# Kernel optimization log

Hardware: AMD Instinct MI355X
Metric: run time of the kernel (lower is better)

The kernel has to match this reference:

```python
import jax, jax.numpy as jnp
import numpy as np


def _gru_cell(x, h, wih, whh, bih, bhh):
    """PyTorch GRUCell semantics. x:[B,2] h:[B,2] wih/whh:[6,2] bih/bhh:[6]."""
    gi = x @ wih.T + bih  # [B,6]
    gh = h @ whh.T + bhh  # [B,6]
    i_r, i_z, i_n = jnp.split(gi, 3, axis=1)
    h_r, h_z, h_n = jnp.split(gh, 3, axis=1)
    r = jax.nn.sigmoid(i_r + h_r)
    z = jax.nn.sigmoid(i_z + h_z)
    n = jnp.tanh(i_n + r * h_n)
    return (1.0 - z) * n + z * h


def setup_inputs() -> dict:
    key = jax.random.key(0)
    ks = jax.random.split(key, 13)
    B = 1048576
    s = 0.5  # small init scale for stable gates
    return {
        "x": jax.random.normal(ks[0], (B, 19), dtype=jnp.float32),
        "up_wih": jax.random.normal(ks[1], (6, 2), dtype=jnp.float32) * s,
        "up_whh": jax.random.normal(ks[2], (6, 2), dtype=jnp.float32) * s,
        "up_bih": jax.random.normal(ks[3], (6,), dtype=jnp.float32) * s,
        "up_bhh": jax.random.normal(ks[4], (6,), dtype=jnp.float32) * s,
        "down_wih": jax.random.normal(ks[5], (6, 2), dtype=jnp.float32) * s,
        "down_whh": jax.random.normal(ks[6], (6, 2), dtype=jnp.float32) * s,
        "down_bih": jax.random.normal(ks[7], (6,), dtype=jnp.float32) * s,
        "down_bhh": jax.random.normal(ks[8], (6,), dtype=jnp.float32) * s,
        "obs_w": jax.random.normal(ks[9], (2, 7), dtype=jnp.float32) * s,
        "obs_b": jax.random.normal(ks[10], (2,), dtype=jnp.float32) * s,
        "out_w": jax.random.normal(ks[11], (1, 2), dtype=jnp.float32) * s,
        "out_b": jax.random.normal(ks[12], (1,), dtype=jnp.float32) * s,
    }


def reference(x, up_wih, up_whh, up_bih, up_bhh,
              down_wih, down_whh, down_bih, down_bhh,
              obs_w, obs_b, out_w, out_b):
    B = x.shape[0]
    obs = x[:, :5]                       # [B,5]
    j = x[:, 5:12]                       # [B,7]
    jd = x[:, 12:19]                     # [B,7]
    jcat = jnp.stack([j, jd], axis=-1)   # [B,7,2] per-joint (pos, vel)
    steps = jnp.swapaxes(jcat, 0, 1)     # [7,B,2]

    # up pass: scan r_up over the 7 joints, collecting hidden states
    h0 = jnp.zeros((B, 2), dtype=x.dtype)

    def up_step(h, inp):
        h_new = _gru_cell(inp, h, up_wih, up_whh, up_bih, up_bhh)
        return h_new, h_new

    h_last, h_up = jax.lax.scan(up_step, h0, steps)  # h_up: [7,B,2]

    # mix observation with final up hidden state
    h = jnp.concatenate([obs, h_last], axis=1) @ obs_w.T + obs_b  # [B,2]

    # down pass: scan r_down over stored up states, emitting actions
    def down_step(h, hu):
        h_new = _gru_cell(hu, h, down_wih, down_whh, down_bih, down_bhh)
        act = h_new @ out_w.T + out_b  # [B,1]
        return h_new, act

    _, acts = jax.lax.scan(down_step, h, h_up)  # [7,B,1]
    return jnp.swapaxes(acts, 0, 1)  # [B,7,1]
```

## Files before the change

kernel.cpp:

```cpp
#include <hip/hip_runtime.h>

#define TPB 256
#define RPB 512

__device__ __forceinline__ float ex2(float x) { return __builtin_amdgcn_exp2f(x); }
__device__ __forceinline__ float frcp(float x) { return __builtin_amdgcn_rcpf(x); }

__device__ __forceinline__ float sigm(float x) {
  return frcp(1.0f + ex2(-1.4426950408889634f * x));
}
__device__ __forceinline__ float ftanh(float x) {
  return fmaf(-2.0f, frcp(ex2(2.8853900817779268f * x) + 1.0f), 1.0f);
}

struct GruW {
  float w0, w1, w2, w3, w4, w5, w6, w7, w8, w9, w10, w11;
  float u0, u1, u2, u3, u4, u5, u6, u7, u8, u9, u10, u11;
  float br0, br1, bz0, bz1;
  float bin0, bin1, bhn0, bhn1;
};

__device__ __forceinline__ GruW load_gru(const float* __restrict__ wih,
                                         const float* __restrict__ whh,
                                         const float* __restrict__ bih,
                                         const float* __restrict__ bhh) {
  GruW g;
  g.w0 = wih[0];  g.w1 = wih[1];  g.w2 = wih[2];  g.w3 = wih[3];
  g.w4 = wih[4];  g.w5 = wih[5];  g.w6 = wih[6];  g.w7 = wih[7];
  g.w8 = wih[8];  g.w9 = wih[9];  g.w10 = wih[10]; g.w11 = wih[11];
  g.u0 = whh[0];  g.u1 = whh[1];  g.u2 = whh[2];  g.u3 = whh[3];
  g.u4 = whh[4];  g.u5 = whh[5];  g.u6 = whh[6];  g.u7 = whh[7];
  g.u8 = whh[8];  g.u9 = whh[9];  g.u10 = whh[10]; g.u11 = whh[11];
  g.br0 = bih[0] + bhh[0]; g.br1 = bih[1] + bhh[1];
  g.bz0 = bih[2] + bhh[2]; g.bz1 = bih[3] + bhh[3];
  g.bin0 = bih[4]; g.bin1 = bih[5];
  g.bhn0 = bhh[4]; g.bhn1 = bhh[5];
  return g;
}

__device__ __forceinline__ void cell(const GruW& g, float x0, float x1,
                                     float& h0, float& h1) {
  float r0 = sigm(fmaf(g.w0, x0, fmaf(g.w1, x1, fmaf(g.u0, h0, fmaf(g.u1, h1, g.br0)))));
  float r1 = sigm(fmaf(g.w2, x0, fmaf(g.w3, x1, fmaf(g.u2, h0, fmaf(g.u3, h1, g.br1)))));
  float z0 = sigm(fmaf(g.w4, x0, fmaf(g.w5, x1, fmaf(g.u4, h0, fmaf(g.u5, h1, g.bz0)))));
  float z1 = sigm(fmaf(g.w6, x0, fmaf(g.w7, x1, fmaf(g.u6, h0, fmaf(g.u7, h1, g.bz1)))));
  float gin0 = fmaf(g.w8, x0, fmaf(g.w9, x1, g.bin0));
  float gin1 = fmaf(g.w10, x0, fmaf(g.w11, x1, g.bin1));
  float ghn0 = fmaf(g.u8, h0, fmaf(g.u9, h1, g.bhn0));
  float ghn1 = fmaf(g.u10, h0, fmaf(g.u11, h1, g.bhn1));
  float n0 = ftanh(fmaf(r0, ghn0, gin0));
  float n1 = ftanh(fmaf(r1, ghn1, gin1));
  h0 = fmaf(z0, h0 - n0, n0);
  h1 = fmaf(z1, h1 - n1, n1);
}

__device__ __forceinline__ void row_compute(
    const float* __restrict__ xr, const GruW& up, const GruW& dn,
    float ow0, float ow1, float ow2, float ow3, float ow4, float ow5, float ow6,
    float ow7, float ow8, float ow9, float ow10, float ow11, float ow12, float ow13,
    float ob0, float ob1, float vw0, float vw1, float vb,
    float& o0, float& o1, float& o2, float& o3, float& o4, float& o5, float& o6) {
  float h0 = 0.f, h1 = 0.f;
  float hu0, hu1, hu2, hu3, hu4, hu5, hu6, hu7, hu8, hu9, hu10, hu11, hu12, hu13;
  cell(up, xr[5],  xr[12], h0, h1); hu0 = h0;  hu1 = h1;
  cell(up, xr[6],  xr[13], h0, h1); hu2 = h0;  hu3 = h1;
  cell(up, xr[7],  xr[14], h0, h1); hu4 = h0;  hu5 = h1;
  cell(up, xr[8],  xr[15], h0, h1); hu6 = h0;  hu7 = h1;
  cell(up, xr[9],  xr[16], h0, h1); hu8 = h0;  hu9 = h1;
  cell(up, xr[10], xr[17], h0, h1); hu10 = h0; hu11 = h1;
  cell(up, xr[11], xr[18], h0, h1); hu12 = h0; hu13 = h1;

  float a0 = fmaf(xr[0], ow0, fmaf(xr[1], ow1, fmaf(xr[2], ow2, fmaf(xr[3], ow3,
             fmaf(xr[4], ow4, fmaf(hu12, ow5, fmaf(hu13, ow6, ob0)))))));
  float a1 = fmaf(xr[0], ow7, fmaf(xr[1], ow8, fmaf(xr[2], ow9, fmaf(xr[3], ow10,
             fmaf(xr[4], ow11, fmaf(hu12, ow12, fmaf(hu13, ow13, ob1)))))));
  h0 = a0; h1 = a1;

  cell(dn, hu0,  hu1,  h0, h1); o0 = fmaf(vw0, h0, fmaf(vw1, h1, vb));
  cell(dn, hu2,  hu3,  h0, h1); o1 = fmaf(vw0, h0, fmaf(vw1, h1, vb));
  cell(dn, hu4,  hu5,  h0, h1); o2 = fmaf(vw0, h0, fmaf(vw1, h1, vb));
  cell(dn, hu6,  hu7,  h0, h1); o3 = fmaf(vw0, h0, fmaf(vw1, h1, vb));
  cell(dn, hu8,  hu9,  h0, h1); o4 = fmaf(vw0, h0, fmaf(vw1, h1, vb));
  cell(dn, hu10, hu11, h0, h1); o5 = fmaf(vw0, h0, fmaf(vw1, h1, vb));
  cell(dn, hu12, hu13, h0, h1); o6 = fmaf(vw0, h0, fmaf(vw1, h1, vb));
}

__global__ __launch_bounds__(TPB, 4) void rec_policy_kernel(
    const float* __restrict__ x,
    const float* __restrict__ up_wih, const float* __restrict__ up_whh,
    const float* __restrict__ up_bih, const float* __restrict__ up_bhh,
    const float* __restrict__ down_wih, const float* __restrict__ down_whh,
    const float* __restrict__ down_bih, const float* __restrict__ down_bhh,
    const float* __restrict__ obs_w, const float* __restrict__ obs_b,
    const float* __restrict__ out_w, const float* __restrict__ out_b,
    float* __restrict__ out, int B) {
  __shared__ __align__(16) float sx[RPB * 19];

  const int tid = threadIdx.x;
  const long base = (long)blockIdx.x * RPB;
  const int rows = min((long)RPB, (long)B - base);

  const GruW up = load_gru(up_wih, up_whh, up_bih, up_bhh);
  const GruW dn = load_gru(down_wih, down_whh, down_bih, down_bhh);
  const float ow0 = obs_w[0], ow1 = obs_w[1], ow2 = obs_w[2], ow3 = obs_w[3],
              ow4 = obs_w[4], ow5 = obs_w[5], ow6 = obs_w[6], ow7 = obs_w[7],
              ow8 = obs_w[8], ow9 = obs_w[9], ow10 = obs_w[10], ow11 = obs_w[11],
              ow12 = obs_w[12], ow13 = obs_w[13];
  const float ob0 = obs_b[0], ob1 = obs_b[1];
  const float vw0 = out_w[0], vw1 = out_w[1], vb = out_b[0];

  if (rows == RPB) {
    {
      const float4* src = (const float4*)(x + base * 19);
      float4* dst = (float4*)sx;
      for (int i = tid; i < RPB * 19 / 4; i += TPB) dst[i] = src[i];
    }
    __syncthreads();

    const float* xa = sx + tid * 19;
    const float* xb = sx + (tid + TPB) * 19;
    float ao0, ao1, ao2, ao3, ao4, ao5, ao6;
    float bo0, bo1, bo2, bo3, bo4, bo5, bo6;
    row_compute(xa, up, dn, ow0, ow1, ow2, ow3, ow4, ow5, ow6, ow7, ow8, ow9,
                ow10, ow11, ow12, ow13, ob0, ob1, vw0, vw1, vb,
                ao0, ao1, ao2, ao3, ao4, ao5, ao6);
    row_compute(xb, up, dn, ow0, ow1, ow2, ow3, ow4, ow5, ow6, ow7, ow8, ow9,
                ow10, ow11, ow12, ow13, ob0, ob1, vw0, vw1, vb,
                bo0, bo1, bo2, bo3, bo4, bo5, bo6);

    __syncthreads();
    float* soa = sx + tid * 7;
    soa[0] = ao0; soa[1] = ao1; soa[2] = ao2; soa[3] = ao3;
    soa[4] = ao4; soa[5] = ao5; soa[6] = ao6;
    float* sob = sx + (tid + TPB) * 7;
    sob[0] = bo0; sob[1] = bo1; sob[2] = bo2; sob[3] = bo3;
    sob[4] = bo4; sob[5] = bo5; sob[6] = bo6;
    __syncthreads();

    float4* dst = (float4*)(out + base * 7);
    const float4* s4 = (const float4*)sx;
    for (int i = tid; i < RPB * 7 / 4; i += TPB) dst[i] = s4[i];
  } else {
    for (int i = tid; i < rows * 19; i += TPB) sx[i] = x[base * 19 + i];
    __syncthreads();
    for (int r = tid; r < rows; r += TPB) {
      const float* xr = sx + r * 19;
      float o0, o1, o2, o3, o4, o5, o6;
      row_compute(xr, up, dn, ow0, ow1, ow2, ow3, ow4, ow5, ow6, ow7, ow8, ow9,
                  ow10, ow11, ow12, ow13, ob0, ob1, vw0, vw1, vb,
                  o0, o1, o2, o3, o4, o5, o6);
      float* po = out + (base + r) * 7;
      po[0] = o0; po[1] = o1; po[2] = o2; po[3] = o3;
      po[4] = o4; po[5] = o5; po[6] = o6;
    }
  }
}

extern "C" void kernel_launch(void* const* d_in, const int* in_sizes, int n_in,
                              void* d_out, int out_size, void* d_ws, size_t ws_size,
                              hipStream_t stream) {
  const float* x        = (const float*)d_in[0];
  const float* up_wih   = (const float*)d_in[1];
  const float* up_whh   = (const float*)d_in[2];
  const float* up_bih   = (const float*)d_in[3];
  const float* up_bhh   = (const float*)d_in[4];
  const float* down_wih = (const float*)d_in[5];
  const float* down_whh = (const float*)d_in[6];
  const float* down_bih = (const float*)d_in[7];
  const float* down_bhh = (const float*)d_in[8];
  const float* obs_w    = (const float*)d_in[9];
  const float* obs_b    = (const float*)d_in[10];
  const float* out_w    = (const float*)d_in[11];
  const float* out_b    = (const float*)d_in[12];
  float* out = (float*)d_out;

  const int B = in_sizes[0] / 19;
  const int blocks = (B + RPB - 1) / RPB;
  rec_policy_kernel<<<blocks, TPB, 0, stream>>>(
      x, up_wih, up_whh, up_bih, up_bhh, down_wih, down_whh, down_bih, down_bhh,
      obs_w, obs_b, out_w, out_b, out, B);
}
```

Measured before the change: 156.1 us.

## Drop shared-memory staging; one row per thread with direct global loads

Removes the LDS staging of input rows and outputs, along with the block barriers. Each thread now handles a single row and reads its 19 floats straight from global memory with strided scalar loads, then writes its 7 outputs directly. The launch bound is raised to 8 blocks per CU and the grid doubles. This trades coalesced float4 transfers for uncoalesced strided accesses that depend on the caches, in exchange for fewer barriers and higher occupancy.

Result: no change. 156.3 us (+0.1%).

```diff
diff --git a/kernel.cpp b/kernel.cpp
--- a/kernel.cpp
+++ b/kernel.cpp
@@ -1,7 +1,6 @@
 #include <hip/hip_runtime.h>
 
 #define TPB 256
-#define RPB 512
 
 __device__ __forceinline__ float ex2(float x) { return __builtin_amdgcn_exp2f(x); }
 __device__ __forceinline__ float frcp(float x) { return __builtin_amdgcn_rcpf(x); }
@@ -54,38 +53,7 @@
   h1 = fmaf(z1, h1 - n1, n1);
 }
 
-__device__ __forceinline__ void row_compute(
-    const float* __restrict__ xr, const GruW& up, const GruW& dn,
-    float ow0, float ow1, float ow2, float ow3, float ow4, float ow5, float ow6,
-    float ow7, float ow8, float ow9, float ow10, float ow11, float ow12, float ow13,
-    float ob0, float ob1, float vw0, float vw1, float vb,
-    float& o0, float& o1, float& o2, float& o3, float& o4, float& o5, float& o6) {
-  float h0 = 0.f, h1 = 0.f;
-  float hu0, hu1, hu2, hu3, hu4, hu5, hu6, hu7, hu8, hu9, hu10, hu11, hu12, hu13;
-  cell(up, xr[5],  xr[12], h0, h1); hu0 = h0;  hu1 = h1;
-  cell(up, xr[6],  xr[13], h0, h1); hu2 = h0;  hu3 = h1;
-  cell(up, xr[7],  xr[14], h0, h1); hu4 = h0;  hu5 = h1;
-  cell(up, xr[8],  xr[15], h0, h1); hu6 = h0;  hu7 = h1;
-  cell(up, xr[9],  xr[16], h0, h1); hu8 = h0;  hu9 = h1;
-  cell(up, xr[10], xr[17], h0, h1); hu10 = h0; hu11 = h1;
-  cell(up, xr[11], xr[18], h0, h1); hu12 = h0; hu13 = h1;
-
-  float a0 = fmaf(xr[0], ow0, fmaf(xr[1], ow1, fmaf(xr[2], ow2, fmaf(xr[3], ow3,
-             fmaf(xr[4], ow4, fmaf(hu12, ow5, fmaf(hu13, ow6, ob0)))))));
-  float a1 = fmaf(xr[0], ow7, fmaf(xr[1], ow8, fmaf(xr[2], ow9, fmaf(xr[3], ow10,
-             fmaf(xr[4], ow11, fmaf(hu12, ow12, fmaf(hu13, ow13, ob1)))))));
-  h0 = a0; h1 = a1;
-
-  cell(dn, hu0,  hu1,  h0, h1); o0 = fmaf(vw0, h0, fmaf(vw1, h1, vb));
-  cell(dn, hu2,  hu3,  h0, h1); o1 = fmaf(vw0, h0, fmaf(vw1, h1, vb));
-  cell(dn, hu4,  hu5,  h0, h1); o2 = fmaf(vw0, h0, fmaf(vw1, h1, vb));
-  cell(dn, hu6,  hu7,  h0, h1); o3 = fmaf(vw0, h0, fmaf(vw1, h1, vb));
-  cell(dn, hu8,  hu9,  h0, h1); o4 = fmaf(vw0, h0, fmaf(vw1, h1, vb));
-  cell(dn, hu10, hu11, h0, h1); o5 = fmaf(vw0, h0, fmaf(vw1, h1, vb));
-  cell(dn, hu12, hu13, h0, h1); o6 = fmaf(vw0, h0, fmaf(vw1, h1, vb));
-}
-
-__global__ __launch_bounds__(TPB, 4) void rec_policy_kernel(
+__global__ __launch_bounds__(TPB, 8) void rec_policy_kernel(
     const float* __restrict__ x,
     const float* __restrict__ up_wih, const float* __restrict__ up_whh,
     const float* __restrict__ up_bih, const float* __restrict__ up_bhh,
@@ -94,11 +62,8 @@
     const float* __restrict__ obs_w, const float* __restrict__ obs_b,
     const float* __restrict__ out_w, const float* __restrict__ out_b,
     float* __restrict__ out, int B) {
-  __shared__ __align__(16) float sx[RPB * 19];
-
-  const int tid = threadIdx.x;
-  const long base = (long)blockIdx.x * RPB;
-  const int rows = min((long)RPB, (long)B - base);
+  const long row = (long)blockIdx.x * TPB + threadIdx.x;
+  if (row >= B) return;
 
   const GruW up = load_gru(up_wih, up_whh, up_bih, up_bhh);
   const GruW dn = load_gru(down_wih, down_whh, down_bih, down_bhh);
@@ -109,51 +74,39 @@
   const float ob0 = obs_b[0], ob1 = obs_b[1];
   const float vw0 = out_w[0], vw1 = out_w[1], vb = out_b[0];
 
-  if (rows == RPB) {
-    {
-      const float4* src = (const float4*)(x + base * 19);
-      float4* dst = (float4*)sx;
-      for (int i = tid; i < RPB * 19 / 4; i += TPB) dst[i] = src[i];
-    }
-    __syncthreads();
+  const float* __restrict__ xp = x + row * 19;
+  float xr0 = xp[0],  xr1 = xp[1],  xr2 = xp[2],  xr3 = xp[3],  xr4 = xp[4];
+  float xr5 = xp[5],  xr6 = xp[6],  xr7 = xp[7],  xr8 = xp[8],  xr9 = xp[9];
+  float xr10 = xp[10], xr11 = xp[11], xr12 = xp[12], xr13 = xp[13];
+  float xr14 = xp[14], xr15 = xp[15], xr16 = xp[16], xr17 = xp[17], xr18 = xp[18];
 
-    const float* xa = sx + tid * 19;
-    const float* xb = sx + (tid + TPB) * 19;
-    float ao0, ao1, ao2, ao3, ao4, ao5, ao6;
-    float bo0, bo1, bo2, bo3, bo4, bo5, bo6;
-    row_compute(xa, up, dn, ow0, ow1, ow2, ow3, ow4, ow5, ow6, ow7, ow8, ow9,
-                ow10, ow11, ow12, ow13, ob0, ob1, vw0, vw1, vb,
-                ao0, ao1, ao2, ao3, ao4, ao5, ao6);
-    row_compute(xb, up, dn, ow0, ow1, ow2, ow3, ow4, ow5, ow6, ow7, ow8, ow9,
-                ow10, ow11, ow12, ow13, ob0, ob1, vw0, vw1, vb,
-                bo0, bo1, bo2, bo3, bo4, bo5, bo6);
+  float h0 = 0.f, h1 = 0.f;
+  float hu0, hu1, hu2, hu3, hu4, hu5, hu6, hu7, hu8, hu9, hu10, hu11, hu12, hu13;
+  cell(up, xr5,  xr12, h0, h1); hu0 = h0;  hu1 = h1;
+  cell(up, xr6,  xr13, h0, h1); hu2 = h0;  hu3 = h1;
+  cell(up, xr7,  xr14, h0, h1); hu4 = h0;  hu5 = h1;
+  cell(up, xr8,  xr15, h0, h1); hu6 = h0;  hu7 = h1;
+  cell(up, xr9,  xr16, h0, h1); hu8 = h0;  hu9 = h1;
+  cell(up, xr10, xr17, h0, h1); hu10 = h0; hu11 = h1;
+  cell(up, xr11, xr18, h0, h1); hu12 = h0; hu13 = h1;
 
-    __syncthreads();
-    float* soa = sx + tid * 7;
-    soa[0] = ao0; soa[1] = ao1; soa[2] = ao2; soa[3] = ao3;
-    soa[4] = ao4; soa[5] = ao5; soa[6] = ao6;
-    float* sob = sx + (tid + TPB) * 7;
-    sob[0] = bo0; sob[1] = bo1; sob[2] = bo2; sob[3] = bo3;
-    sob[4] = bo4; sob[5] = bo5; sob[6] = bo6;
-    __syncthreads();
+  float a0 = fmaf(xr0, ow0, fmaf(xr1, ow1, fmaf(xr2, ow2, fmaf(xr3, ow3,
+             fmaf(xr4, ow4, fmaf(hu12, ow5, fmaf(hu13, ow6, ob0)))))));
+  float a1 = fmaf(xr0, ow7, fmaf(xr1, ow8, fmaf(xr2, ow9, fmaf(xr3, ow10,
+             fmaf(xr4, ow11, fmaf(hu12, ow12, fmaf(hu13, ow13, ob1)))))));
+  h0 = a0; h1 = a1;
 
-    float4* dst = (float4*)(out + base * 7);
-    const float4* s4 = (const float4*)sx;
-    for (int i = tid; i < RPB * 7 / 4; i += TPB) dst[i] = s4[i];
-  } else {
-    for (int i = tid; i < rows * 19; i += TPB) sx[i] = x[base * 19 + i];
-    __syncthreads();
-    for (int r = tid; r < rows; r += TPB) {
-      const float* xr = sx + r * 19;
-      float o0, o1, o2, o3, o4, o5, o6;
-      row_compute(xr, up, dn, ow0, ow1, ow2, ow3, ow4, ow5, ow6, ow7, ow8, ow9,
-                  ow10, ow11, ow12, ow13, ob0, ob1, vw0, vw1, vb,
-                  o0, o1, o2, o3, o4, o5, o6);
-      float* po = out + (base + r) * 7;
-      po[0] = o0; po[1] = o1; po[2] = o2; po[3] = o3;
-      po[4] = o4; po[5] = o5; po[6] = o6;
-    }
-  }
+  float* __restrict__ po = out + row * 7;
+  float o0, o1, o2, o3, o4, o5, o6;
+  cell(dn, hu0,  hu1,  h0, h1); o0 = fmaf(vw0, h0, fmaf(vw1, h1, vb));
+  cell(dn, hu2,  hu3,  h0, h1); o1 = fmaf(vw0, h0, fmaf(vw1, h1, vb));
+  cell(dn, hu4,  hu5,  h0, h1); o2 = fmaf(vw0, h0, fmaf(vw1, h1, vb));
+  cell(dn, hu6,  hu7,  h0, h1); o3 = fmaf(vw0, h0, fmaf(vw1, h1, vb));
+  cell(dn, hu8,  hu9,  h0, h1); o4 = fmaf(vw0, h0, fmaf(vw1, h1, vb));
+  cell(dn, hu10, hu11, h0, h1); o5 = fmaf(vw0, h0, fmaf(vw1, h1, vb));
+  cell(dn, hu12, hu13, h0, h1); o6 = fmaf(vw0, h0, fmaf(vw1, h1, vb));
+  po[0] = o0; po[1] = o1; po[2] = o2; po[3] = o3;
+  po[4] = o4; po[5] = o5; po[6] = o6;
 }
 
 extern "C" void kernel_launch(void* const* d_in, const int* in_sizes, int n_in,
@@ -175,7 +128,7 @@
   float* out = (float*)d_out;
 
   const int B = in_sizes[0] / 19;
-  const int blocks = (B + RPB - 1) / RPB;
+  const int blocks = (B + TPB - 1) / TPB;
   rec_policy_kernel<<<blocks, TPB, 0, stream>>>(
       x, up_wih, up_whh, up_bih, up_bhh, down_wih, down_whh, down_bih, down_bhh,
       obs_w, obs_b, out_w, out_b, out, B);
```
